# Performance work log

Hardware: AMD Instinct MI355X
Metric: run time of the kernel (lower is better)

## Reference

```python
import jax, jax.numpy as jnp
import numpy as np

# Central first difference with zero (same) padding along `axis`:
# out[i] = f[i+1] - f[i-1], zeros outside the domain (conv3d w/ [-1,0,1] kernel, same pad).
def d1(f, axis):
    pad = [(0, 0)] * f.ndim
    pad[axis] = (1, 1)
    fp = jnp.pad(f, pad)
    hi = tuple(slice(2, None) if a == axis else slice(None) for a in range(f.ndim))
    lo = tuple(slice(None, -2) if a == axis else slice(None) for a in range(f.ndim))
    return fp[hi] - fp[lo]

# Second difference: f[i+1] - 2 f[i] + f[i-1], zero padded.
def d2(f, axis):
    pad = [(0, 0)] * f.ndim
    pad[axis] = (1, 1)
    fp = jnp.pad(f, pad)
    hi = tuple(slice(2, None) if a == axis else slice(None) for a in range(f.ndim))
    lo = tuple(slice(None, -2) if a == axis else slice(None) for a in range(f.ndim))
    return fp[hi] - 2.0 * f + fp[lo]

AX_T, AX_X, AX_Y = 2, 3, 4  # [B, C, T, X, Y]
D_t = lambda f: d1(f, AX_T)
D_x = lambda f: d1(f, AX_X)
D_y = lambda f: d1(f, AX_Y)
D_xx_yy = lambda f: d2(f, AX_X) + d2(f, AX_Y)  # Laplacian in x,y


def setup_inputs() -> dict:
    key = jax.random.key(0)
    B, C, T, X, Y = 8, 4, 64, 128, 128
    vars_ = jax.random.normal(key, (B, C, T, X, Y), dtype=jnp.float32)
    return {
        "vars": vars_,
        "dx": jnp.float32(0.0078),
        "dt": jnp.float32(0.05),
        "eta": jnp.float32(0.01),
        "zeta": jnp.float32(0.01),
    }


def reference(vars, dx, dt, eta, zeta):
    rho = vars[:, 0:1]
    u = vars[:, 1:2]
    v = vars[:, 2:3]
    p = vars[:, 3:4]

    # mass residual (final, rescaled assignment in the torch source;
    # `self.rho` there is the continuity-eq density field rho)
    mass = (D_t(rho) * dx
            + rho * (D_x(u) + D_y(v)) * dt
            + u * D_x(rho) * dt
            + v * D_y(rho) * dt)

    div = D_x(u) + D_y(v)
    bulk = zeta + eta / 3.0

    mom_x = (rho * D_t(u) * 2.0 * dx ** 2
             + u * D_x(u) * 2.0 * dt * dx
             + v * D_y(u) * 2.0 * dt * dx
             + D_x(p) * 2.0 * dt * dx
             - eta * D_xx_yy(u) * 4.0 * dt
             - bulk * D_x(div) * 2.0 * dt)
    mom_y = (rho * D_t(v) * 2.0 * dx ** 2
             + u * D_x(v) * 2.0 * dt * dx
             + v * D_y(v) * 2.0 * dt * dx
             + D_y(p) * 2.0 * dt * dx
             - eta * D_xx_yy(v) * 4.0 * dt
             - bulk * D_y(div) * 2.0 * dt)
    mom = mom_x + mom_y

    # boundary=False path: strip 1-cell boundary in t, x, y; stack residuals on channel
    inner = (Ellipsis, slice(1, -1), slice(1, -1), slice(1, -1))
    return jnp.concatenate([mass[inner], mom[inner]], axis=1)
```

## Files before the change

kernel.cpp:

```cpp
#include <hip/hip_runtime.h>


typedef float vf4 __attribute__((ext_vector_type(4)));
typedef float vf4u __attribute__((ext_vector_type(4), aligned(4)));

__device__ __forceinline__ vf4 ld4(const float* __restrict__ p) {
    return *reinterpret_cast<const vf4u*>(p);
}

struct Win { vf4 lo, hi; };
#define SH(w, s) __builtin_shufflevector((w).lo, (w).hi, 2 + (s), 3 + (s), 4 + (s), 5 + (s))

__device__ __forceinline__ Win mkwin(vf4 c, float mHi) {
    const float dn0 = __shfl_down(c.x, 1) * mHi;
    const float dn1 = __shfl_down(c.y, 1) * mHi;
    Win w;
    w.lo = (vf4){0.0f, c.x, c.y, c.z};
    w.hi = (vf4){c.w, dn0, dn1, 0.0f};
    return w;
}

__device__ __forceinline__ Win mkwin2(vf4 c, float mLo, float mHi) {
    const float up3 = __shfl_up(c.w, 1) * mLo;
    const float dn0 = __shfl_down(c.x, 1) * mHi;
    const float dn1 = __shfl_down(c.y, 1) * mHi;
    const float dn2 = __shfl_down(c.z, 1) * mHi;
    Win w;
    w.lo = (vf4){up3, c.x, c.y, c.z};
    w.hi = (vf4){c.w, dn0, dn1, dn2};
    return w;
}

__global__ __launch_bounds__(256) void cns_residuals_kernel(
    const float* __restrict__ vars,
    const float* __restrict__ s_dx, const float* __restrict__ s_dt,
    const float* __restrict__ s_eta, const float* __restrict__ s_zeta,
    float* __restrict__ out)
{
    const float dx = s_dx[0], dt = s_dt[0], eta = s_eta[0], zeta = s_zeta[0];
    const float bulk = zeta + eta * (1.0f / 3.0f);
    const float c1 = 2.0f * dx * dx;
    const float c2 = 2.0f * dt * dx;
    const float c3 = 4.0f * dt;
    const float c4 = 2.0f * dt;

    const int i = blockIdx.x;
    const int xcd = i & 7;
    const int slot = i >> 3;
    const int lb = ((xcd < 4) ? xcd * 977 : 3908 + (xcd - 4) * 976) + slot;

    const int tid = lb * 256 + threadIdx.x;
    const int j = tid & 31;
    int r = tid >> 5;
    const int xp = r % 126; r /= 126;
    const int tp = r % 62;  const int b = r / 62;
    const int x = xp + 1, t = tp + 1;
    const int yb = 1 + 4 * j;
    const int q = 4 * j;

    const size_t plane = 16384;
    const size_t cstr  = (size_t)64 * plane;

    const float* baseA = vars + (size_t)b * 4 * cstr + (size_t)t * plane
                       + ((size_t)x << 7);
    const float* Rrow = baseA;
    const float* Urow = baseA + cstr;
    const float* Vrow = baseA + 2 * cstr;
    const float* Prow = baseA + 3 * cstr;

    const float mLo = (j == 0)  ? 0.0f : 1.0f;
    const float mHi = (j == 31) ? 0.0f : 1.0f;

    const Win Rw0 = mkwin(ld4(Rrow + q), mHi);
    const Win Uwm = mkwin(ld4(Urow - 128 + q), mHi);
    const Win Uw0 = mkwin(ld4(Urow + q), mHi);
    const Win Uw1 = mkwin(ld4(Urow + 128 + q), mHi);
    const Win Vwm = mkwin(ld4(Vrow - 128 + q), mHi);
    const Win Vw0 = mkwin2(ld4(Vrow + q), mLo, mHi);
    const Win Vw1 = mkwin(ld4(Vrow + 128 + q), mHi);
    const Win Pw0 = mkwin(ld4(Prow + q), mHi);

    const float* R0 = Rrow + yb;
    const float* U0 = Urow + yb;
    const float* V0 = Vrow + yb;
    const float* P0 = Prow + yb;
    const vf4 rxp = ld4(R0 + 128), rxm = ld4(R0 - 128);
    const vf4 rtp = ld4(R0 + plane), rtm = ld4(R0 - plane);
    const vf4 utp = ld4(U0 + plane), utm = ld4(U0 - plane);
    const vf4 vtp = ld4(V0 + plane), vtm = ld4(V0 - plane);
    const vf4 pxp = ld4(P0 + 128), pxm = ld4(P0 - 128);
    const vf4 zero = {0.0f, 0.0f, 0.0f, 0.0f};
    const vf4 uxp2 = (x <= 125) ? ld4(U0 + 256) : zero;
    const vf4 uxm2 = (x >= 2)   ? ld4(U0 - 256) : zero;

    const vf4 rho = SH(Rw0, 0);
    const vf4 u   = SH(Uw0, 0);
    const vf4 v   = SH(Vw0, 0);

    const vf4 uxp = SH(Uw1, 0), uxm = SH(Uwm, 0);
    const vf4 uyp = SH(Uw0, 1), uym = SH(Uw0, -1);
    const vf4 vxp = SH(Vw1, 0), vxm = SH(Vwm, 0);
    const vf4 vyp = SH(Vw0, 1), vym = SH(Vw0, -1);

    const vf4 Dt_rho = rtp - rtm;
    const vf4 Dx_rho = rxp - rxm;
    const vf4 Dy_rho = SH(Rw0, 1) - SH(Rw0, -1);
    const vf4 Dx_u = uxp - uxm, Dy_u = uyp - uym;
    const vf4 Dx_v = vxp - vxm, Dy_v = vyp - vym;

    const vf4 mass = Dt_rho * dx + rho * (Dx_u + Dy_v) * dt
                   + u * Dx_rho * dt + v * Dy_rho * dt;

    const vf4 Dt_u = utp - utm, Dt_v = vtp - vtm;
    const vf4 Dx_p = pxp - pxm;
    const vf4 Dy_p = SH(Pw0, 1) - SH(Pw0, -1);
    const vf4 lap_u = uxp + uxm + uyp + uym - 4.0f * u;
    const vf4 lap_v = vxp + vxm + vyp + vym - 4.0f * v;

    const vf4 Dx_div = uxp2 - 2.0f * u + uxm2
                     + SH(Vw1, 1) - SH(Vw1, -1)
                     - SH(Vwm, 1) + SH(Vwm, -1);
    const vf4 Dy_div = SH(Vw0, 2) - 2.0f * v + SH(Vw0, -2)
                     + SH(Uw1, 1) - SH(Uwm, 1)
                     - SH(Uw1, -1) + SH(Uwm, -1);

    const vf4 mom = rho * (Dt_u + Dt_v) * c1
                  + (u * (Dx_u + Dx_v) + v * (Dy_u + Dy_v)) * c2
                  + (Dx_p + Dy_p) * c2
                  - eta * (lap_u + lap_v) * c3
                  - bulk * (Dx_div + Dy_div) * c4;

    const size_t oplane = 126 * 126;
    const size_t ocstr  = (size_t)62 * oplane;
    float* o1 = out + (size_t)b * 2 * ocstr + (size_t)tp * oplane
              + (size_t)xp * 126 + 4 * j;
    float* o2 = o1 + ocstr;
    if (j < 31) {
        __builtin_nontemporal_store(mass, reinterpret_cast<vf4u*>(o1));
        __builtin_nontemporal_store(mom,  reinterpret_cast<vf4u*>(o2));
    } else {
        __builtin_nontemporal_store(mass[0], o1);
        __builtin_nontemporal_store(mass[1], o1 + 1);
        __builtin_nontemporal_store(mom[0],  o2);
        __builtin_nontemporal_store(mom[1],  o2 + 1);
    }
}

extern "C" void kernel_launch(void* const* d_in, const int* in_sizes, int n_in,
                              void* d_out, int out_size, void* d_ws, size_t ws_size,
                              hipStream_t stream) {
    const float* vars   = (const float*)d_in[0];
    const float* s_dx   = (const float*)d_in[1];
    const float* s_dt   = (const float*)d_in[2];
    const float* s_eta  = (const float*)d_in[3];
    const float* s_zeta = (const float*)d_in[4];
    float* out = (float*)d_out;

    const int grid = 7812;
    hipLaunchKernelGGL(cns_residuals_kernel, dim3(grid), dim3(256), 0, stream,
                       vars, s_dx, s_dt, s_eta, s_zeta, out);
}
```

Baseline: 37.12 us.

## Stage x-row tiles of all channels in LDS for 14-row blocks

Reorganizes the kernel so each 448-thread block handles 14 consecutive x rows of one (b,t) plane. It cooperatively loads the needed rows of rho, u, v and p, including x halos and zero padding, into shared memory. Neighbour x-row reads then come from LDS instead of repeated global loads, while the t-neighbour loads still go to global memory. This adds a block barrier, about 33KB of LDS per block, and a new grid mapping with an XCD-aware block index.

New measurement: 116.9 us. 215% more time.

```diff
diff --git a/kernel.cpp b/kernel.cpp
--- a/kernel.cpp
+++ b/kernel.cpp
@@ -4,7 +4,7 @@
 typedef float vf4 __attribute__((ext_vector_type(4)));
 typedef float vf4u __attribute__((ext_vector_type(4), aligned(4)));
 
-__device__ __forceinline__ vf4 ld4(const float* __restrict__ p) {
+__device__ __forceinline__ vf4 ld4(const float* p) {
     return *reinterpret_cast<const vf4u*>(p);
 }
 
@@ -19,7 +19,6 @@
     w.hi = (vf4){c.w, dn0, dn1, 0.0f};
     return w;
 }
-
 __device__ __forceinline__ Win mkwin2(vf4 c, float mLo, float mHi) {
     const float up3 = __shfl_up(c.w, 1) * mLo;
     const float dn0 = __shfl_down(c.x, 1) * mHi;
@@ -30,13 +29,19 @@
     w.hi = (vf4){c.w, dn0, dn1, dn2};
     return w;
 }
+__device__ __forceinline__ vf4 ctr(vf4 c, float mHi) {
+    const float dn0 = __shfl_down(c.x, 1) * mHi;
+    return (vf4){c.y, c.z, c.w, dn0};
+}
 
-__global__ __launch_bounds__(256) void cns_residuals_kernel(
+__global__ __launch_bounds__(448, 7) void cns_residuals_kernel(
     const float* __restrict__ vars,
     const float* __restrict__ s_dx, const float* __restrict__ s_dt,
     const float* __restrict__ s_eta, const float* __restrict__ s_zeta,
     float* __restrict__ out)
 {
+    __shared__ float lds[66 * 128];
+
     const float dx = s_dx[0], dt = s_dt[0], eta = s_eta[0], zeta = s_zeta[0];
     const float bulk = zeta + eta * (1.0f / 3.0f);
     const float c1 = 2.0f * dx * dx;
@@ -45,53 +50,70 @@
     const float c4 = 2.0f * dt;
 
     const int i = blockIdx.x;
-    const int xcd = i & 7;
-    const int slot = i >> 3;
-    const int lb = ((xcd < 4) ? xcd * 977 : 3908 + (xcd - 4) * 976) + slot;
+    const int lb = (i & 7) * 558 + (i >> 3);
+    int r = lb;
+    const int xg = r % 9; r /= 9;
+    const int tp = r % 62; const int b = r / 62;
+    const int xp0 = xg * 14;
+    const int x0 = xp0 + 1;
+    const int t = tp + 1;
 
-    const int tid = lb * 256 + threadIdx.x;
-    const int j = tid & 31;
-    int r = tid >> 5;
-    const int xp = r % 126; r /= 126;
-    const int tp = r % 62;  const int b = r / 62;
-    const int x = xp + 1, t = tp + 1;
-    const int yb = 1 + 4 * j;
-    const int q = 4 * j;
+    const int j  = threadIdx.x & 31;
+    const int xl = threadIdx.x >> 5;
+    const int q  = 4 * j;
 
     const size_t plane = 16384;
     const size_t cstr  = (size_t)64 * plane;
+    const float* cbase = vars + (size_t)b * 4 * cstr + (size_t)t * plane;
 
-    const float* baseA = vars + (size_t)b * 4 * cstr + (size_t)t * plane
-                       + ((size_t)x << 7);
-    const float* Rrow = baseA;
-    const float* Urow = baseA + cstr;
-    const float* Vrow = baseA + 2 * cstr;
-    const float* Prow = baseA + 3 * cstr;
+    for (int c = threadIdx.x; c < 66 * 32; c += 448) {
+        const int sr = c >> 5;
+        const int cw = c & 31;
+        int ch, grow;
+        if (sr < 16)      { ch = 0; grow = x0 - 1 + sr; }
+        else if (sr < 34) { ch = 1; grow = x0 - 2 + (sr - 16); }
+        else if (sr < 50) { ch = 2; grow = x0 - 1 + (sr - 34); }
+        else              { ch = 3; grow = x0 - 1 + (sr - 50); }
+        vf4 val = {0.0f, 0.0f, 0.0f, 0.0f};
+        if ((unsigned)grow < 128u)
+            val = ld4(cbase + (size_t)ch * cstr + ((size_t)grow << 7) + 4 * cw);
+        *reinterpret_cast<vf4*>(&lds[sr * 128 + 4 * cw]) = val;
+    }
+    __syncthreads();
 
     const float mLo = (j == 0)  ? 0.0f : 1.0f;
     const float mHi = (j == 31) ? 0.0f : 1.0f;
 
-    const Win Rw0 = mkwin(ld4(Rrow + q), mHi);
-    const Win Uwm = mkwin(ld4(Urow - 128 + q), mHi);
-    const Win Uw0 = mkwin(ld4(Urow + q), mHi);
-    const Win Uw1 = mkwin(ld4(Urow + 128 + q), mHi);
-    const Win Vwm = mkwin(ld4(Vrow - 128 + q), mHi);
-    const Win Vw0 = mkwin2(ld4(Vrow + q), mLo, mHi);
-    const Win Vw1 = mkwin(ld4(Vrow + 128 + q), mHi);
-    const Win Pw0 = mkwin(ld4(Prow + q), mHi);
+    const float* LR = &lds[(xl + 1) * 128 + q];
+    const float* LU = &lds[(16 + xl + 2) * 128 + q];
+    const float* LV = &lds[(34 + xl + 1) * 128 + q];
+    const float* LP = &lds[(50 + xl + 1) * 128 + q];
 
-    const float* R0 = Rrow + yb;
-    const float* U0 = Urow + yb;
-    const float* V0 = Vrow + yb;
-    const float* P0 = Prow + yb;
-    const vf4 rxp = ld4(R0 + 128), rxm = ld4(R0 - 128);
-    const vf4 rtp = ld4(R0 + plane), rtm = ld4(R0 - plane);
-    const vf4 utp = ld4(U0 + plane), utm = ld4(U0 - plane);
-    const vf4 vtp = ld4(V0 + plane), vtm = ld4(V0 - plane);
-    const vf4 pxp = ld4(P0 + 128), pxm = ld4(P0 - 128);
-    const vf4 zero = {0.0f, 0.0f, 0.0f, 0.0f};
-    const vf4 uxp2 = (x <= 125) ? ld4(U0 + 256) : zero;
-    const vf4 uxm2 = (x >= 2)   ? ld4(U0 - 256) : zero;
+    const vf4 cR   = ld4(LR);
+    const vf4 cRp  = ld4(LR + 128), cRm  = ld4(LR - 128);
+    const vf4 cU   = ld4(LU);
+    const vf4 cUp  = ld4(LU + 128), cUm  = ld4(LU - 128);
+    const vf4 cUp2 = ld4(LU + 256), cUm2 = ld4(LU - 256);
+    const vf4 cV   = ld4(LV);
+    const vf4 cVp  = ld4(LV + 128), cVm  = ld4(LV - 128);
+    const vf4 cP   = ld4(LP);
+    const vf4 cPp  = ld4(LP + 128), cPm  = ld4(LP - 128);
+
+    const int x = x0 + xl;
+    const float* gb = cbase + ((size_t)x << 7) + (q + 1);
+    const vf4 rtp = ld4(gb + plane),             rtm = ld4(gb - plane);
+    const vf4 utp = ld4(gb + cstr + plane),      utm = ld4(gb + cstr - plane);
+    const vf4 vtp = ld4(gb + 2 * cstr + plane),  vtm = ld4(gb + 2 * cstr - plane);
+
+    const Win Rw0 = mkwin(cR, mHi);
+    const Win Uw0 = mkwin(cU, mHi);
+    const Win Uwm = mkwin(cUm, mHi), Uw1 = mkwin(cUp, mHi);
+    const Win Vw0 = mkwin2(cV, mLo, mHi);
+    const Win Vwm = mkwin(cVm, mHi), Vw1 = mkwin(cVp, mHi);
+    const Win Pw0 = mkwin(cP, mHi);
+    const vf4 rxp = ctr(cRp, mHi), rxm = ctr(cRm, mHi);
+    const vf4 pxp = ctr(cPp, mHi), pxm = ctr(cPm, mHi);
+    const vf4 uxp2 = ctr(cUp2, mHi), uxm2 = ctr(cUm2, mHi);
 
     const vf4 rho = SH(Rw0, 0);
     const vf4 u   = SH(Uw0, 0);
@@ -132,6 +154,7 @@
 
     const size_t oplane = 126 * 126;
     const size_t ocstr  = (size_t)62 * oplane;
+    const int xp = xp0 + xl;
     float* o1 = out + (size_t)b * 2 * ocstr + (size_t)tp * oplane
               + (size_t)xp * 126 + 4 * j;
     float* o2 = o1 + ocstr;
@@ -156,7 +179,7 @@
     const float* s_zeta = (const float*)d_in[4];
     float* out = (float*)d_out;
 
-    const int grid = 7812;
-    hipLaunchKernelGGL(cns_residuals_kernel, dim3(grid), dim3(256), 0, stream,
+    const int grid = 4464;
+    hipLaunchKernelGGL(cns_residuals_kernel, dim3(grid), dim3(448), 0, stream,
                        vars, s_dx, s_dt, s_eta, s_zeta, out);
 }
```

## Share x-neighbor rows between paired half-waves via cross-lane swaps

Applied to the files above, without the earlier changes.

Pairs the two 32-lane halves of each wave, which work on adjacent x rows, so each half loads only one neighbor row per field and gets the other from its partner through __shfl_xor(…,32). Signed x-differences are assembled using a per-half sign factor folded into the coefficients. The goal is fewer global/L2 vector loads per output row. The cost is extra cross-lane shuffles and more arithmetic. It also relies on paired halves holding x and x±1 within the same t and b, which the row indexing appears to assume.

New measurement: 36.26 us (median of 2 runs). -2.3%, faster.

```diff
diff --git a/kernel.cpp b/kernel.cpp
--- a/kernel.cpp
+++ b/kernel.cpp
@@ -4,7 +4,7 @@
 typedef float vf4 __attribute__((ext_vector_type(4)));
 typedef float vf4u __attribute__((ext_vector_type(4), aligned(4)));
 
-__device__ __forceinline__ vf4 ld4(const float* __restrict__ p) {
+__device__ __forceinline__ vf4 ld4(const float* p) {
     return *reinterpret_cast<const vf4u*>(p);
 }
 
@@ -19,7 +19,6 @@
     w.hi = (vf4){c.w, dn0, dn1, 0.0f};
     return w;
 }
-
 __device__ __forceinline__ Win mkwin2(vf4 c, float mLo, float mHi) {
     const float up3 = __shfl_up(c.w, 1) * mLo;
     const float dn0 = __shfl_down(c.x, 1) * mHi;
@@ -29,6 +28,18 @@
     w.lo = (vf4){up3, c.x, c.y, c.z};
     w.hi = (vf4){c.w, dn0, dn1, dn2};
     return w;
+}
+__device__ __forceinline__ vf4 ctrf(vf4 c, float mHi) {
+    const float dn0 = __shfl_down(c.x, 1) * mHi;
+    return (vf4){c.y, c.z, c.w, dn0};
+}
+__device__ __forceinline__ vf4 swap4(vf4 c) {
+    vf4 r;
+    r.x = __shfl_xor(c.x, 32);
+    r.y = __shfl_xor(c.y, 32);
+    r.z = __shfl_xor(c.z, 32);
+    r.w = __shfl_xor(c.w, 32);
+    return r;
 }
 
 __global__ __launch_bounds__(256) void cns_residuals_kernel(
@@ -43,6 +54,7 @@
     const float c2 = 2.0f * dt * dx;
     const float c3 = 4.0f * dt;
     const float c4 = 2.0f * dt;
+    const float bc4 = bulk * c4;
 
     const int i = blockIdx.x;
     const int xcd = i & 7;
@@ -55,85 +67,106 @@
     const int xp = r % 126; r /= 126;
     const int tp = r % 62;  const int b = r / 62;
     const int x = xp + 1, t = tp + 1;
-    const int yb = 1 + 4 * j;
     const int q = 4 * j;
+    const int h = (threadIdx.x >> 5) & 1;
+
+    const float ssgn = h ? -1.0f : 1.0f;
+    const float dts  = dt * ssgn;
+    const float c2s  = c2 * ssgn;
+    const float bc4s = bc4 * ssgn;
 
     const size_t plane = 16384;
     const size_t cstr  = (size_t)64 * plane;
 
-    const float* baseA = vars + (size_t)b * 4 * cstr + (size_t)t * plane
-                       + ((size_t)x << 7);
-    const float* Rrow = baseA;
-    const float* Urow = baseA + cstr;
-    const float* Vrow = baseA + 2 * cstr;
-    const float* Prow = baseA + 3 * cstr;
+    const float* Rch = vars + (size_t)b * 4 * cstr + (size_t)t * plane;
+    const float* Uch = Rch + cstr;
+    const float* Vch = Rch + 2 * cstr;
+    const float* Pch = Rch + 3 * cstr;
+
+    const int xe = x + 2 * h - 1;
+    const int xo = x + 4 * h - 2;
+
+    const vf4 R_c = ld4(Rch + ((size_t)x  << 7) + q);
+    const vf4 R_e = ld4(Rch + ((size_t)xe << 7) + q);
+    const vf4 U_c = ld4(Uch + ((size_t)x  << 7) + q);
+    const vf4 U_i = ld4(Uch + ((size_t)xe << 7) + q);
+    vf4 U_o = {0.0f, 0.0f, 0.0f, 0.0f};
+    if ((unsigned)xo < 128u) U_o = ld4(Uch + ((size_t)xo << 7) + q);
+    const vf4 V_c = ld4(Vch + ((size_t)x  << 7) + q);
+    const vf4 V_e = ld4(Vch + ((size_t)xe << 7) + q);
+    const vf4 P_c = ld4(Pch + ((size_t)x  << 7) + q);
+    const vf4 P_e = ld4(Pch + ((size_t)xe << 7) + q);
+
+    const float* rowR = Rch + ((size_t)x << 7) + q + 1;
+    const vf4 rtp = ld4(rowR + plane),            rtm = ld4(rowR - plane);
+    const vf4 utp = ld4(rowR + cstr + plane),     utm = ld4(rowR + cstr - plane);
+    const vf4 vtp = ld4(rowR + 2 * cstr + plane), vtm = ld4(rowR + 2 * cstr - plane);
 
     const float mLo = (j == 0)  ? 0.0f : 1.0f;
     const float mHi = (j == 31) ? 0.0f : 1.0f;
 
-    const Win Rw0 = mkwin(ld4(Rrow + q), mHi);
-    const Win Uwm = mkwin(ld4(Urow - 128 + q), mHi);
-    const Win Uw0 = mkwin(ld4(Urow + q), mHi);
-    const Win Uw1 = mkwin(ld4(Urow + 128 + q), mHi);
-    const Win Vwm = mkwin(ld4(Vrow - 128 + q), mHi);
-    const Win Vw0 = mkwin2(ld4(Vrow + q), mLo, mHi);
-    const Win Vw1 = mkwin(ld4(Vrow + 128 + q), mHi);
-    const Win Pw0 = mkwin(ld4(Prow + q), mHi);
+    const vf4 Rcs = swap4(R_c);
+    const vf4 Pcs = swap4(P_c);
+    const vf4 Ucs = swap4(U_c);
+    const vf4 Uis = swap4(U_i);
+    const vf4 Vcs = swap4(V_c);
 
-    const float* R0 = Rrow + yb;
-    const float* U0 = Urow + yb;
-    const float* V0 = Vrow + yb;
-    const float* P0 = Prow + yb;
-    const vf4 rxp = ld4(R0 + 128), rxm = ld4(R0 - 128);
-    const vf4 rtp = ld4(R0 + plane), rtm = ld4(R0 - plane);
-    const vf4 utp = ld4(U0 + plane), utm = ld4(U0 - plane);
-    const vf4 vtp = ld4(V0 + plane), vtm = ld4(V0 - plane);
-    const vf4 pxp = ld4(P0 + 128), pxm = ld4(P0 - 128);
-    const vf4 zero = {0.0f, 0.0f, 0.0f, 0.0f};
-    const vf4 uxp2 = (x <= 125) ? ld4(U0 + 256) : zero;
-    const vf4 uxm2 = (x >= 2)   ? ld4(U0 - 256) : zero;
+    const Win Rw  = mkwin(R_c, mHi);
+    const Win Pw  = mkwin(P_c, mHi);
+    const Win Uw0 = mkwin(U_c, mHi);
+    const Win Vw0 = mkwin2(V_c, mLo, mHi);
+    const Win Au  = mkwin(U_i, mHi);
+    const Win Bu  = mkwin(Ucs, mHi);
+    const Win Av  = mkwin(V_e, mHi);
+    const Win Bv  = mkwin(Vcs, mHi);
 
-    const vf4 rho = SH(Rw0, 0);
+    const vf4 rho = SH(Rw, 0);
     const vf4 u   = SH(Uw0, 0);
     const vf4 v   = SH(Vw0, 0);
-
-    const vf4 uxp = SH(Uw1, 0), uxm = SH(Uwm, 0);
     const vf4 uyp = SH(Uw0, 1), uym = SH(Uw0, -1);
-    const vf4 vxp = SH(Vw1, 0), vxm = SH(Vwm, 0);
     const vf4 vyp = SH(Vw0, 1), vym = SH(Vw0, -1);
 
+    const vf4 au = SH(Au, 0), bu = SH(Bu, 0);
+    const vf4 av = SH(Av, 0), bv = SH(Bv, 0);
+    const vf4 sum_ux = au + bu;
+    const vf4 sum_vx = av + bv;
+    const vf4 rawDx_u = bu - au;
+    const vf4 rawDx_v = bv - av;
+
+    const vf4 rawDx_rho = ctrf(Rcs - R_e, mHi);
+    const vf4 rawDx_p   = ctrf(Pcs - P_e, mHi);
+    const vf4 usum2     = ctrf(U_o + Uis, mHi);
+
+    const vf4 Dy_rho = SH(Rw, 1) - SH(Rw, -1);
+    const vf4 Dy_p   = SH(Pw, 1) - SH(Pw, -1);
+    const vf4 Dy_u   = uyp - uym;
+    const vf4 Dy_v   = vyp - vym;
+
+    const vf4 lap_u = sum_ux + uyp + uym - 4.0f * u;
+    const vf4 lap_v = sum_vx + vyp + vym - 4.0f * v;
+
+    const vf4 unsignedDiv = (usum2 - 2.0f * u)
+                          + (SH(Vw0, 2) - 2.0f * v + SH(Vw0, -2));
+    const vf4 signedDiv = (SH(Bv, 1) - SH(Bv, -1)) - (SH(Av, 1) - SH(Av, -1))
+                        + (SH(Bu, 1) - SH(Bu, -1)) - (SH(Au, 1) - SH(Au, -1));
+
     const vf4 Dt_rho = rtp - rtm;
-    const vf4 Dx_rho = rxp - rxm;
-    const vf4 Dy_rho = SH(Rw0, 1) - SH(Rw0, -1);
-    const vf4 Dx_u = uxp - uxm, Dy_u = uyp - uym;
-    const vf4 Dx_v = vxp - vxm, Dy_v = vyp - vym;
+    const vf4 Dt_u = utp - utm, Dt_v = vtp - vtm;
 
-    const vf4 mass = Dt_rho * dx + rho * (Dx_u + Dy_v) * dt
-                   + u * Dx_rho * dt + v * Dy_rho * dt;
-
-    const vf4 Dt_u = utp - utm, Dt_v = vtp - vtm;
-    const vf4 Dx_p = pxp - pxm;
-    const vf4 Dy_p = SH(Pw0, 1) - SH(Pw0, -1);
-    const vf4 lap_u = uxp + uxm + uyp + uym - 4.0f * u;
-    const vf4 lap_v = vxp + vxm + vyp + vym - 4.0f * v;
-
-    const vf4 Dx_div = uxp2 - 2.0f * u + uxm2
-                     + SH(Vw1, 1) - SH(Vw1, -1)
-                     - SH(Vwm, 1) + SH(Vwm, -1);
-    const vf4 Dy_div = SH(Vw0, 2) - 2.0f * v + SH(Vw0, -2)
-                     + SH(Uw1, 1) - SH(Uwm, 1)
-                     - SH(Uw1, -1) + SH(Uwm, -1);
+    const vf4 mass = Dt_rho * dx
+                   + (rho * rawDx_u + u * rawDx_rho) * dts
+                   + (rho * Dy_v + v * Dy_rho) * dt;
 
     const vf4 mom = rho * (Dt_u + Dt_v) * c1
-                  + (u * (Dx_u + Dx_v) + v * (Dy_u + Dy_v)) * c2
-                  + (Dx_p + Dy_p) * c2
+                  + (u * (rawDx_u + rawDx_v) + rawDx_p) * c2s
+                  + (v * (Dy_u + Dy_v) + Dy_p) * c2
                   - eta * (lap_u + lap_v) * c3
-                  - bulk * (Dx_div + Dy_div) * c4;
+                  - bc4 * unsignedDiv - bc4s * signedDiv;
 
     const size_t oplane = 126 * 126;
     const size_t ocstr  = (size_t)62 * oplane;
     float* o1 = out + (size_t)b * 2 * ocstr + (size_t)tp * oplane
-              + (size_t)xp * 126 + 4 * j;
+              + (size_t)xp * 126 + q;
     float* o2 = o1 + ocstr;
     if (j < 31) {
         __builtin_nontemporal_store(mass, reinterpret_cast<vf4u*>(o1));
```
